# Kernel tuning notes

Hardware: AMD Instinct MI355X
Metric: run time of the kernel (lower is better)

Reference implementation:

```python
import jax, jax.numpy as jnp
import numpy as np

V, D, T, H, L, NC = 50257, 1024, 512, 16, 4, 3
HS = D // H  # head size 64
DFF = 4 * D
B = 16


def _ln(x, g, b, eps=1e-5):
    mu = jnp.mean(x, axis=-1, keepdims=True)
    var = jnp.var(x, axis=-1, keepdims=True)
    return (x - mu) * jax.lax.rsqrt(var + eps) * g + b


def setup_inputs() -> dict:
    key = jax.random.key(0)
    ks = jax.random.split(key, 20)
    s = 0.02
    inp = {
        "x": jax.random.randint(ks[0], (B, T), 0, V),
        "tok_emb": jax.random.normal(ks[1], (V, D), jnp.float32) * s,
        "pos_emb": jax.random.normal(ks[2], (T, D), jnp.float32) * s,
        "Wq": jax.random.normal(ks[3], (L, H, D, HS), jnp.float32) * s,
        "Wk": jax.random.normal(ks[4], (L, H, D, HS), jnp.float32) * s,
        "Wv": jax.random.normal(ks[5], (L, H, D, HS), jnp.float32) * s,
        "Wproj": jax.random.normal(ks[6], (L, H * HS, D), jnp.float32) * s,
        "bproj": jnp.zeros((L, D), jnp.float32),
        "ln1_g": jnp.ones((L, D), jnp.float32),
        "ln1_b": jnp.zeros((L, D), jnp.float32),
        "ln2_g": jnp.ones((L, D), jnp.float32),
        "ln2_b": jnp.zeros((L, D), jnp.float32),
        "W1": jax.random.normal(ks[7], (L, D, DFF), jnp.float32) * s,
        "b1": jnp.zeros((L, DFF), jnp.float32),
        "W2": jax.random.normal(ks[8], (L, DFF, D), jnp.float32) * s,
        "b2": jnp.zeros((L, D), jnp.float32),
        "lnf_g": jnp.ones((D,), jnp.float32),
        "lnf_b": jnp.zeros((D,), jnp.float32),
        "Wout": jax.random.normal(ks[9], (T * D, NC), jnp.float32) * s,
        "bout": jnp.zeros((NC,), jnp.float32),
    }
    return inp


def reference(x, tok_emb, pos_emb, Wq, Wk, Wv, Wproj, bproj, ln1_g, ln1_b,
              ln2_g, ln2_b, W1, b1, W2, b2, lnf_g, lnf_b, Wout, bout):
    Bx, Tx = x.shape
    h = tok_emb[x] + pos_emb[:Tx]  # [B,T,D]; dropout=identity (eval)
    scale = HS ** -0.5
    for l in range(L):
        z = _ln(h, ln1_g[l], ln1_b[l])
        q = jnp.einsum('btd,hde->bhte', z, Wq[l])
        k = jnp.einsum('btd,hde->bhte', z, Wk[l])
        v = jnp.einsum('btd,hde->bhte', z, Wv[l])
        att = jax.nn.softmax(jnp.einsum('bhte,bhse->bhts', q, k) * scale, axis=-1)
        o = jnp.einsum('bhts,bhse->bhte', att, v)  # [B,H,T,HS]
        o = o.transpose(0, 2, 1, 3).reshape(Bx, Tx, H * HS)
        h = h + o @ Wproj[l] + bproj[l]
        z2 = _ln(h, ln2_g[l], ln2_b[l])
        ffn = jax.nn.gelu(z2 @ W1[l] + b1[l], approximate=False) @ W2[l] + b2[l]
        h = h + ffn
    h = _ln(h, lnf_g, lnf_b)
    logits = h.reshape(Bx, -1) @ Wout + bout  # [B,NC]
    return logits
```

## Files before the change

kernel.cpp:

```cpp
#include <hip/hip_runtime.h>
#include <math.h>
#include <stdint.h>

#define DEV __device__ __forceinline__

constexpr int Bz = 16, T = 512, D = 1024, H = 16, HS = 64, Lx = 4, DFF = 4096, NCn = 3;
constexpr int BT = Bz * T;
constexpr long QSZ = (long)Bz * H * T * HS;

typedef __attribute__((ext_vector_type(8))) short v8s;
typedef __attribute__((ext_vector_type(4))) float v4f;

DEV uint16_t f2bf(float f) {
  uint32_t u = __float_as_uint(f);
  u += 0x7fff + ((u >> 16) & 1);
  return (uint16_t)(u >> 16);
}

DEV void async_copy16(const void* g, void* l) {
  __builtin_amdgcn_global_load_lds(
      (const __attribute__((address_space(1))) uint32_t*)g,
      (__attribute__((address_space(3))) uint32_t*)l, 16, 0, 0);
}

__global__ void transpose_cast_kernel(const float* __restrict__ in, uint16_t* __restrict__ out,
                                      int R, int C, long s1, long s2, int zdiv) {
  __shared__ float tile[32][33];
  int zz = blockIdx.z;
  in += (long)zz * R * C;
  out += (long)(zz / zdiv) * s1 + (long)(zz % zdiv) * s2;
  int c0 = blockIdx.x * 32, r0 = blockIdx.y * 32;
  int tx = threadIdx.x, ty = threadIdx.y;
  for (int i = 0; i < 32; i += 8)
    tile[ty + i][tx] = in[(long)(r0 + ty + i) * C + (c0 + tx)];
  __syncthreads();
  for (int i = 0; i < 32; i += 8)
    out[(long)(c0 + ty + i) * R + (r0 + tx)] = f2bf(tile[tx][ty + i]);
}

__global__ void embed_kernel(const int* __restrict__ x, const float* __restrict__ tok,
                             const float* __restrict__ pos, float* __restrict__ h) {
  int row = blockIdx.x;
  int t = row & (T - 1);
  int id = x[row];
  const float4* tr = (const float4*)(tok + (long)id * D);
  const float4* pr = (const float4*)(pos + (long)t * D);
  float4* hr = (float4*)(h + (long)row * D);
  int i = threadIdx.x;
  float4 a = tr[i], b = pr[i];
  hr[i] = make_float4(a.x + b.x, a.y + b.y, a.z + b.z, a.w + b.w);
}

template <bool OUT_BF16>
__global__ void ln_kernel(const float* __restrict__ in, const float* __restrict__ g,
                          const float* __restrict__ b, void* __restrict__ out) {
  int row = blockIdx.x;
  int i = threadIdx.x;
  const float4* xr = (const float4*)(in + (long)row * D);
  float4 v = xr[i];
  float s = v.x + v.y + v.z + v.w;
  float s2 = v.x * v.x + v.y * v.y + v.z * v.z + v.w * v.w;
  for (int off = 32; off; off >>= 1) { s += __shfl_down(s, off); s2 += __shfl_down(s2, off); }
  __shared__ float sh1[4], sh2[4];
  int wid = i >> 6, lane = i & 63;
  if (lane == 0) { sh1[wid] = s; sh2[wid] = s2; }
  __syncthreads();
  s = sh1[0] + sh1[1] + sh1[2] + sh1[3];
  s2 = sh2[0] + sh2[1] + sh2[2] + sh2[3];
  float mu = s * (1.0f / D);
  float rstd = rsqrtf(s2 * (1.0f / D) - mu * mu + 1e-5f);
  float4 gv = ((const float4*)g)[i];
  float4 bv = ((const float4*)b)[i];
  float o0 = (v.x - mu) * rstd * gv.x + bv.x;
  float o1 = (v.y - mu) * rstd * gv.y + bv.y;
  float o2 = (v.z - mu) * rstd * gv.z + bv.z;
  float o3 = (v.w - mu) * rstd * gv.w + bv.w;
  if constexpr (OUT_BF16) {
    uint16_t* orow = (uint16_t*)out + (long)row * D;
    orow[4 * i + 0] = f2bf(o0); orow[4 * i + 1] = f2bf(o1);
    orow[4 * i + 2] = f2bf(o2); orow[4 * i + 3] = f2bf(o3);
  } else {
    ((float4*)((float*)out + (long)row * D))[i] = make_float4(o0, o1, o2, o3);
  }
}

__global__ void softmax_kernel(uint16_t* __restrict__ S) {
  int wid = threadIdx.x >> 6, lane = threadIdx.x & 63;
  long row = (long)blockIdx.x * 4 + wid;
  uint4* p = (uint4*)(S + row * T) + lane;
  uint4 u = *p;
  uint32_t w[4] = {u.x, u.y, u.z, u.w};
  float lo[4], hi[4];
  float m = -1e30f;
#pragma unroll
  for (int i = 0; i < 4; i++) {
    lo[i] = __uint_as_float(w[i] << 16) * 0.125f;
    hi[i] = __uint_as_float(w[i] & 0xffff0000u) * 0.125f;
    m = fmaxf(m, fmaxf(lo[i], hi[i]));
  }
  for (int off = 32; off; off >>= 1) m = fmaxf(m, __shfl_xor(m, off));
  float s = 0.f;
#pragma unroll
  for (int i = 0; i < 4; i++) {
    lo[i] = expf(lo[i] - m); hi[i] = expf(hi[i] - m);
    s += lo[i] + hi[i];
  }
  for (int off = 32; off; off >>= 1) s += __shfl_xor(s, off);
  float inv = 1.0f / s;
  uint4 o;
  uint32_t* ow = (uint32_t*)&o;
#pragma unroll
  for (int i = 0; i < 4; i++)
    ow[i] = (uint32_t)f2bf(lo[i] * inv) | ((uint32_t)f2bf(hi[i] * inv) << 16);
  *p = o;
}

enum { MQKV = 0, MBF = 1, MO = 2, MATOMIC = 3, MGELU = 4 };

template <int BM, int BN, int WGM, int WGN, int MODE>
__global__ void gemm_kernel(const uint16_t* __restrict__ A, const uint16_t* __restrict__ Bt,
                            int M, int N, int K, int lda, int ldb,
                            long strideA, long strideB, long strideC,
                            const float* __restrict__ bias, void* __restrict__ Cout) {
  constexpr int WM = BM / WGM, WN = BN / WGN;
  constexpr int TM = WM / 16, TN = WN / 16;
  __shared__ __align__(16) uint16_t As[2][BM * 32];
  __shared__ __align__(16) uint16_t Bs[2][BN * 32];
  int kz = 0, batch = 0;
  if constexpr (MODE == MATOMIC) kz = blockIdx.z; else batch = blockIdx.z;
  A += (long)batch * strideA;
  Bt += (long)batch * strideB;
  const int kb0 = kz * K;
  int bm0 = blockIdx.x * BM, bn0 = blockIdx.y * BN;
  int tid = threadIdx.x, wid = tid >> 6, lane = tid & 63;
  int wm = wid / WGN, wn = wid % WGN;
  v4f acc[TM][TN] = {};

  const int laneRow = lane >> 2;
  const int laneB = ((lane & 3) ^ ((laneRow >> 1) & 3)) * 16;
  const int rl = lane & 15;
  const int cx16 = (rl * 4 + ((lane >> 4) ^ ((rl >> 1) & 3))) * 16;

  for (int k0 = kb0; k0 < kb0 + K; k0 += 64) {
    __syncthreads();
#pragma unroll
    for (int p = 0; p < 2; p++) {
      for (int c = wid; c < BM / 16; c += 4) {
        int row = bm0 + c * 16 + laneRow;
        async_copy16((const char*)(A + (long)row * lda + k0 + p * 32) + laneB,
                     (char*)As[p] + c * 1024);
      }
      for (int c = wid; c < BN / 16; c += 4) {
        int col = bn0 + c * 16 + laneRow;
        async_copy16((const char*)(Bt + (long)col * ldb + k0 + p * 32) + laneB,
                     (char*)Bs[p] + c * 1024);
      }
    }
    __syncthreads();

#pragma unroll
    for (int p = 0; p < 2; p++) {
      v8s af[TM], bfr[TN];
#pragma unroll
      for (int i = 0; i < TM; i++)
        af[i] = *(const v8s*)((const char*)As[p] + (wm * (WM / 16) + i) * 1024 + cx16);
#pragma unroll
      for (int j = 0; j < TN; j++)
        bfr[j] = *(const v8s*)((const char*)Bs[p] + (wn * (WN / 16) + j) * 1024 + cx16);
#pragma unroll
      for (int i = 0; i < TM; i++)
#pragma unroll
        for (int j = 0; j < TN; j++)
          acc[i][j] = __builtin_amdgcn_mfma_f32_16x16x32_bf16(af[i], bfr[j], acc[i][j], 0, 0, 0);
    }
  }

#pragma unroll
  for (int i = 0; i < TM; i++) {
    int row0 = bm0 + wm * WM + i * 16 + (lane >> 4) * 4;
#pragma unroll
    for (int j = 0; j < TN; j++) {
      int col = bn0 + wn * WN + j * 16 + (lane & 15);
#pragma unroll
      for (int r = 0; r < 4; r++) {
        int row = row0 + r;
        float val = acc[i][j][r];
        if constexpr (MODE == MQKV) {
          int sel = col >> 10, c = col & 1023;
          int hh = c >> 6, e = c & 63;
          int b = row >> 9, t = row & 511;
          long idx = (sel < 2) ? (((long)(b * H + hh) * T + t) * HS + e)
                               : (((long)(b * H + hh) * HS + e) * T + t);
          ((uint16_t*)Cout)[(long)sel * QSZ + idx] = f2bf(val);
        } else if constexpr (MODE == MBF) {
          ((uint16_t*)Cout)[(long)batch * strideC + (long)row * N + col] = f2bf(val);
        } else if constexpr (MODE == MO) {
          int b = batch >> 4, hh = batch & 15;
          ((uint16_t*)Cout)[((long)(b * T + row) * H + hh) * HS + col] = f2bf(val);
        } else if constexpr (MODE == MATOMIC) {
          float add = val + ((kz == 0) ? bias[col] : 0.f);
          atomicAdd(&((float*)Cout)[(long)row * N + col], add);
        } else if constexpr (MODE == MGELU) {
          float xg = val + bias[col];
          float gl = 0.5f * xg * (1.0f + erff(xg * 0.70710678118f));
          ((uint16_t*)Cout)[(long)row * N + col] = f2bf(gl);
        }
      }
    }
  }
}

__global__ void logits_init(const float* __restrict__ bout, float* __restrict__ out) {
  int i = threadIdx.x;
  if (i < Bz * NCn) out[i] = bout[i % NCn];
}
__global__ void logits_kernel(const float* __restrict__ hf, const float* __restrict__ Wout,
                              float* __restrict__ out) {
  int b = blockIdx.y, c = blockIdx.z;
  long base = (long)blockIdx.x * 8192;
  const float* hv = hf + (long)b * T * D + base;
  const float* w = Wout + base * NCn + c;
  float s = 0.f;
  for (int i = threadIdx.x; i < 8192; i += 256) s += hv[i] * w[(long)i * NCn];
  for (int off = 32; off; off >>= 1) s += __shfl_down(s, off);
  __shared__ float sh[4];
  int wid = threadIdx.x >> 6, lane = threadIdx.x & 63;
  if (lane == 0) sh[wid] = s;
  __syncthreads();
  if (threadIdx.x == 0) atomicAdd(out + b * NCn + c, sh[0] + sh[1] + sh[2] + sh[3]);
}

extern "C" void kernel_launch(void* const* d_in, const int* in_sizes, int n_in,
                              void* d_out, int out_size, void* d_ws, size_t ws_size,
                              hipStream_t stream) {
  const int* x = (const int*)d_in[0];
  const float* tok = (const float*)d_in[1];
  const float* pos = (const float*)d_in[2];
  const float* Wq = (const float*)d_in[3];
  const float* Wk = (const float*)d_in[4];
  const float* Wv = (const float*)d_in[5];
  const float* Wproj = (const float*)d_in[6];
  const float* bproj = (const float*)d_in[7];
  const float* ln1g = (const float*)d_in[8];
  const float* ln1b = (const float*)d_in[9];
  const float* ln2g = (const float*)d_in[10];
  const float* ln2b = (const float*)d_in[11];
  const float* W1 = (const float*)d_in[12];
  const float* b1 = (const float*)d_in[13];
  const float* W2 = (const float*)d_in[14];
  const float* b2 = (const float*)d_in[15];
  const float* lnfg = (const float*)d_in[16];
  const float* lnfb = (const float*)d_in[17];
  const float* Wout = (const float*)d_in[18];
  const float* bout = (const float*)d_in[19];
  float* out = (float*)d_out;

  char* ws = (char*)d_ws;
  size_t off = 0;
  auto alloc = [&](size_t bytes) { char* p = ws + off; off += (bytes + 255) & ~(size_t)255; return p; };
  uint16_t* wqkvT = (uint16_t*)alloc((size_t)Lx * 3 * D * D * 2);
  uint16_t* wpT = (uint16_t*)alloc((size_t)Lx * D * D * 2);
  uint16_t* w1T = (uint16_t*)alloc((size_t)Lx * D * DFF * 2);
  uint16_t* w2T = (uint16_t*)alloc((size_t)Lx * D * DFF * 2);
  float* h = (float*)alloc((size_t)BT * D * 4);
  uint16_t* z = (uint16_t*)alloc((size_t)BT * D * 2);
  uint16_t* qkv = (uint16_t*)alloc((size_t)3 * QSZ * 2);
  uint16_t* Sb = (uint16_t*)alloc((size_t)Bz * H * T * T * 2);
  uint16_t* o = (uint16_t*)alloc((size_t)BT * D * 2);
  uint16_t* a1 = (uint16_t*)alloc((size_t)BT * DFF * 2);
  (void)ws_size; (void)in_sizes; (void)n_in; (void)out_size;

  uint16_t* q = qkv;
  uint16_t* kb = qkv + QSZ;
  uint16_t* vt = qkv + 2 * QSZ;

  dim3 tb(32, 8);
  transpose_cast_kernel<<<dim3(HS / 32, D / 32, Lx * H), tb, 0, stream>>>(
      Wq, wqkvT, D, HS, 3L * D * D, (long)HS * D, H);
  transpose_cast_kernel<<<dim3(HS / 32, D / 32, Lx * H), tb, 0, stream>>>(
      Wk, wqkvT + (long)D * D, D, HS, 3L * D * D, (long)HS * D, H);
  transpose_cast_kernel<<<dim3(HS / 32, D / 32, Lx * H), tb, 0, stream>>>(
      Wv, wqkvT + 2L * D * D, D, HS, 3L * D * D, (long)HS * D, H);
  transpose_cast_kernel<<<dim3(D / 32, D / 32, Lx), tb, 0, stream>>>(
      Wproj, wpT, D, D, (long)D * D, 0, 1);
  transpose_cast_kernel<<<dim3(DFF / 32, D / 32, Lx), tb, 0, stream>>>(
      W1, w1T, D, DFF, (long)D * DFF, 0, 1);
  transpose_cast_kernel<<<dim3(D / 32, DFF / 32, Lx), tb, 0, stream>>>(
      W2, w2T, DFF, D, (long)D * DFF, 0, 1);

  embed_kernel<<<BT, 256, 0, stream>>>(x, tok, pos, h);

  for (int l = 0; l < Lx; l++) {
    const uint16_t* wqkv_l = wqkvT + (size_t)l * 3 * D * D;
    const uint16_t* wp_l = wpT + (size_t)l * D * D;
    const uint16_t* w1_l = w1T + (size_t)l * D * DFF;
    const uint16_t* w2_l = w2T + (size_t)l * D * DFF;

    ln_kernel<true><<<BT, 256, 0, stream>>>(h, ln1g + l * D, ln1b + l * D, z);

    gemm_kernel<128, 128, 2, 2, MQKV><<<dim3(BT / 128, 3 * D / 128, 1), 256, 0, stream>>>(
        z, wqkv_l, BT, 3 * D, D, D, D, 0, 0, 0, nullptr, qkv);

    gemm_kernel<128, 128, 2, 2, MBF><<<dim3(T / 128, T / 128, Bz * H), 256, 0, stream>>>(
        q, kb, T, T, HS, HS, HS, (long)T * HS, (long)T * HS, (long)T * T, nullptr, Sb);

    softmax_kernel<<<Bz * H * T / 4, 256, 0, stream>>>(Sb);

    gemm_kernel<128, 64, 4, 1, MO><<<dim3(T / 128, 1, Bz * H), 256, 0, stream>>>(
        Sb, vt, T, HS, T, T, T, (long)T * T, (long)HS * T, 0, nullptr, o);

    gemm_kernel<128, 128, 2, 2, MATOMIC><<<dim3(BT / 128, D / 128, 2), 256, 0, stream>>>(
        o, wp_l, BT, D, D / 2, D, D, 0, 0, 0, bproj + l * D, h);

    ln_kernel<true><<<BT, 256, 0, stream>>>(h, ln2g + l * D, ln2b + l * D, z);

    gemm_kernel<128, 128, 2, 2, MGELU><<<dim3(BT / 128, DFF / 128, 1), 256, 0, stream>>>(
        z, w1_l, BT, DFF, D, D, D, 0, 0, 0, b1 + l * DFF, a1);

    gemm_kernel<128, 128, 2, 2, MATOMIC><<<dim3(BT / 128, D / 128, 2), 256, 0, stream>>>(
        a1, w2_l, BT, D, DFF / 2, DFF, DFF, 0, 0, 0, b2 + l * D, h);
  }

  ln_kernel<false><<<BT, 256, 0, stream>>>(h, lnfg, lnfb, h);
  logits_init<<<1, 64, 0, stream>>>(bout, out);
  logits_kernel<<<dim3(64, Bz, NCn), 256, 0, stream>>>(h, Wout, out);
}
```

Baseline: 2.484 ms.

## Add 256x256 tiled 8-wave GEMM with XCD-aware remap for dense projections

Introduces a new GEMM kernel with 256x256 output tiles and 512 threads per block. It uses double-buffered async global-to-LDS copies with swizzled layout and splits each K-step into four MFMA phases interleaved with prefetch stages and priority hints. Block IDs are remapped so that neighbouring tiles land on the same XCD. The QKV, output projection and both FFN GEMMs now use it, aiming for more data reuse per tile and better L2 locality. The trade-off is a large register and LDS footprint per block and fewer blocks, which may lower occupancy or leave CUs idle on the smaller N=1024 GEMMs.

After: 2.696 ms. +8.6%, slower.

```diff
diff --git a/kernel.cpp b/kernel.cpp
--- a/kernel.cpp
+++ b/kernel.cpp
@@ -185,18 +185,167 @@
       for (int r = 0; r < 4; r++) {
         int row = row0 + r;
         float val = acc[i][j][r];
-        if constexpr (MODE == MQKV) {
-          int sel = col >> 10, c = col & 1023;
-          int hh = c >> 6, e = c & 63;
-          int b = row >> 9, t = row & 511;
-          long idx = (sel < 2) ? (((long)(b * H + hh) * T + t) * HS + e)
-                               : (((long)(b * H + hh) * HS + e) * T + t);
-          ((uint16_t*)Cout)[(long)sel * QSZ + idx] = f2bf(val);
-        } else if constexpr (MODE == MBF) {
+        if constexpr (MODE == MBF) {
           ((uint16_t*)Cout)[(long)batch * strideC + (long)row * N + col] = f2bf(val);
         } else if constexpr (MODE == MO) {
           int b = batch >> 4, hh = batch & 15;
           ((uint16_t*)Cout)[((long)(b * T + row) * H + hh) * HS + col] = f2bf(val);
+        }
+      }
+    }
+  }
+}
+
+template <int MODE>
+__global__ __launch_bounds__(512, 2) void gemm256_kernel(
+    const uint16_t* __restrict__ A, const uint16_t* __restrict__ Bt,
+    int mt, int N, int K, int lda, int ldb,
+    const float* __restrict__ bias, void* __restrict__ Cout) {
+  __shared__ __align__(16) uint16_t lds[8][8192];
+  const int NT = K >> 6;
+  int kz = 0;
+  if constexpr (MODE == MATOMIC) kz = blockIdx.z;
+  const int kb0 = kz * K;
+
+  int nwg = gridDim.x, orig = blockIdx.x;
+  int q = nwg >> 3, r = nwg & 7;
+  int xcd = orig & 7, base = orig >> 3;
+  int wgid = (xcd < r ? xcd * (q + 1) : r * (q + 1) + (xcd - r) * q) + base;
+  int bm0 = (wgid % mt) * 256, bn0 = (wgid / mt) * 256;
+
+  int tid = threadIdx.x, wid = tid >> 6, lane = tid & 63;
+  int wm = wid >> 2, wn = wid & 3;
+
+  const int laneRow = lane >> 2;
+  const int g8 = ((lane & 3) ^ ((laneRow >> 1) & 3)) * 8;
+  const int rl = lane & 15;
+  const int cx16 = (rl * 4 + ((lane >> 4) ^ ((rl >> 1) & 3))) * 16;
+
+  auto stage = [&](int h) {
+    if (h >= 4 * NT) return;
+    int th = h >> 2, part = h & 3;
+    char* slot = (char*)lds[(th & 1) * 4 + part];
+    int k0 = kb0 + th * 64;
+    const uint16_t* src; int ld, r0;
+    if (part < 2) { src = Bt; ld = ldb; r0 = bn0 + part * 128; }
+    else          { src = A;  ld = lda; r0 = bm0 + (part - 2) * 128; }
+#pragma unroll
+    for (int c0 = 0; c0 < 2; c0++) {
+      int c = wid + c0 * 8;
+      int rg = c >> 1, kc = c & 1;
+      async_copy16(src + (long)(r0 + rg * 16 + laneRow) * ld + k0 + kc * 32 + g8,
+                   slot + c * 1024);
+    }
+  };
+
+  v4f acc[8][4] = {};
+
+  for (int h = 0; h < 6; h++) stage(h);
+  asm volatile("s_waitcnt vmcnt(4)" ::: "memory");
+  __builtin_amdgcn_s_barrier();
+
+  for (int t = 0; t < NT; t++) {
+    const char* Aslot = (const char*)lds[(t & 1) * 4 + 2 + wm];
+    const char* Bslot = (const char*)lds[(t & 1) * 4 + (wn >> 1)];
+    const int jb = (wn & 1) * 4;
+    v8s af[4][2], bf0[2][2], bf1[2][2];
+
+#pragma unroll
+    for (int i = 0; i < 4; i++)
+#pragma unroll
+      for (int kc = 0; kc < 2; kc++)
+        af[i][kc] = *(const v8s*)(Aslot + (i * 2 + kc) * 1024 + cx16);
+#pragma unroll
+    for (int j = 0; j < 2; j++)
+#pragma unroll
+      for (int kc = 0; kc < 2; kc++)
+        bf0[j][kc] = *(const v8s*)(Bslot + ((jb + j) * 2 + kc) * 1024 + cx16);
+    stage(4 * t + 6);
+    __builtin_amdgcn_s_barrier();
+    asm volatile("s_waitcnt lgkmcnt(0)" ::: "memory");
+    __builtin_amdgcn_s_setprio(1);
+#pragma unroll
+    for (int i = 0; i < 4; i++)
+#pragma unroll
+      for (int j = 0; j < 2; j++)
+#pragma unroll
+        for (int kc = 0; kc < 2; kc++)
+          acc[i][j] = __builtin_amdgcn_mfma_f32_16x16x32_bf16(af[i][kc], bf0[j][kc], acc[i][j], 0, 0, 0);
+    __builtin_amdgcn_s_setprio(0);
+    __builtin_amdgcn_s_barrier();
+
+#pragma unroll
+    for (int j = 0; j < 2; j++)
+#pragma unroll
+      for (int kc = 0; kc < 2; kc++)
+        bf1[j][kc] = *(const v8s*)(Bslot + ((jb + 2 + j) * 2 + kc) * 1024 + cx16);
+    stage(4 * t + 7);
+    __builtin_amdgcn_s_barrier();
+    asm volatile("s_waitcnt lgkmcnt(0)" ::: "memory");
+    __builtin_amdgcn_s_setprio(1);
+#pragma unroll
+    for (int i = 0; i < 4; i++)
+#pragma unroll
+      for (int j = 0; j < 2; j++)
+#pragma unroll
+        for (int kc = 0; kc < 2; kc++)
+          acc[i][2 + j] = __builtin_amdgcn_mfma_f32_16x16x32_bf16(af[i][kc], bf1[j][kc], acc[i][2 + j], 0, 0, 0);
+    __builtin_amdgcn_s_setprio(0);
+    __builtin_amdgcn_s_barrier();
+
+#pragma unroll
+    for (int i = 0; i < 4; i++)
+#pragma unroll
+      for (int kc = 0; kc < 2; kc++)
+        af[i][kc] = *(const v8s*)(Aslot + ((4 + i) * 2 + kc) * 1024 + cx16);
+    stage(4 * t + 8);
+    __builtin_amdgcn_s_barrier();
+    asm volatile("s_waitcnt lgkmcnt(0)" ::: "memory");
+    __builtin_amdgcn_s_setprio(1);
+#pragma unroll
+    for (int i = 0; i < 4; i++)
+#pragma unroll
+      for (int j = 0; j < 2; j++)
+#pragma unroll
+        for (int kc = 0; kc < 2; kc++)
+          acc[4 + i][2 + j] = __builtin_amdgcn_mfma_f32_16x16x32_bf16(af[i][kc], bf1[j][kc], acc[4 + i][2 + j], 0, 0, 0);
+    __builtin_amdgcn_s_setprio(0);
+    __builtin_amdgcn_s_barrier();
+
+    stage(4 * t + 9);
+    if (t >= NT - 2) asm volatile("s_waitcnt vmcnt(0)" ::: "memory");
+    else             asm volatile("s_waitcnt vmcnt(4)" ::: "memory");
+    __builtin_amdgcn_s_barrier();
+    asm volatile("s_waitcnt lgkmcnt(0)" ::: "memory");
+    __builtin_amdgcn_s_setprio(1);
+#pragma unroll
+    for (int i = 0; i < 4; i++)
+#pragma unroll
+      for (int j = 0; j < 2; j++)
+#pragma unroll
+        for (int kc = 0; kc < 2; kc++)
+          acc[4 + i][j] = __builtin_amdgcn_mfma_f32_16x16x32_bf16(af[i][kc], bf0[j][kc], acc[4 + i][j], 0, 0, 0);
+    __builtin_amdgcn_s_setprio(0);
+    __builtin_amdgcn_s_barrier();
+  }
+
+#pragma unroll
+  for (int i = 0; i < 8; i++) {
+    int row0 = bm0 + wm * 128 + i * 16 + (lane >> 4) * 4;
+#pragma unroll
+    for (int j = 0; j < 4; j++) {
+      int col = bn0 + wn * 64 + j * 16 + rl;
+#pragma unroll
+      for (int r = 0; r < 4; r++) {
+        int row = row0 + r;
+        float val = acc[i][j][r];
+        if constexpr (MODE == MQKV) {
+          int sel = col >> 10, c = col & 1023;
+          int hh = c >> 6, e = c & 63;
+          int b = row >> 9, tt = row & 511;
+          long idx = (sel < 2) ? (((long)(b * H + hh) * T + tt) * HS + e)
+                               : (((long)(b * H + hh) * HS + e) * T + tt);
+          ((uint16_t*)Cout)[(long)sel * QSZ + idx] = f2bf(val);
         } else if constexpr (MODE == MATOMIC) {
           float add = val + ((kz == 0) ? bias[col] : 0.f);
           atomicAdd(&((float*)Cout)[(long)row * N + col], add);
@@ -290,6 +439,8 @@
 
   embed_kernel<<<BT, 256, 0, stream>>>(x, tok, pos, h);
 
+  constexpr int MT = BT / 256;
+
   for (int l = 0; l < Lx; l++) {
     const uint16_t* wqkv_l = wqkvT + (size_t)l * 3 * D * D;
     const uint16_t* wp_l = wpT + (size_t)l * D * D;
@@ -298,8 +449,8 @@
 
     ln_kernel<true><<<BT, 256, 0, stream>>>(h, ln1g + l * D, ln1b + l * D, z);
 
-    gemm_kernel<128, 128, 2, 2, MQKV><<<dim3(BT / 128, 3 * D / 128, 1), 256, 0, stream>>>(
-        z, wqkv_l, BT, 3 * D, D, D, D, 0, 0, 0, nullptr, qkv);
+    gemm256_kernel<MQKV><<<dim3(MT * (3 * D / 256), 1, 1), 512, 0, stream>>>(
+        z, wqkv_l, MT, 3 * D, D, D, D, nullptr, qkv);
 
     gemm_kernel<128, 128, 2, 2, MBF><<<dim3(T / 128, T / 128, Bz * H), 256, 0, stream>>>(
         q, kb, T, T, HS, HS, HS, (long)T * HS, (long)T * HS, (long)T * T, nullptr, Sb);
@@ -309,16 +460,16 @@
     gemm_kernel<128, 64, 4, 1, MO><<<dim3(T / 128, 1, Bz * H), 256, 0, stream>>>(
         Sb, vt, T, HS, T, T, T, (long)T * T, (long)HS * T, 0, nullptr, o);
 
-    gemm_kernel<128, 128, 2, 2, MATOMIC><<<dim3(BT / 128, D / 128, 2), 256, 0, stream>>>(
-        o, wp_l, BT, D, D / 2, D, D, 0, 0, 0, bproj + l * D, h);
+    gemm256_kernel<MATOMIC><<<dim3(MT * (D / 256), 1, 2), 512, 0, stream>>>(
+        o, wp_l, MT, D, D / 2, D, D, bproj + l * D, h);
 
     ln_kernel<true><<<BT, 256, 0, stream>>>(h, ln2g + l * D, ln2b + l * D, z);
 
-    gemm_kernel<128, 128, 2, 2, MGELU><<<dim3(BT / 128, DFF / 128, 1), 256, 0, stream>>>(
-        z, w1_l, BT, DFF, D, D, D, 0, 0, 0, b1 + l * DFF, a1);
-
-    gemm_kernel<128, 128, 2, 2, MATOMIC><<<dim3(BT / 128, D / 128, 2), 256, 0, stream>>>(
-        a1, w2_l, BT, D, DFF / 2, DFF, DFF, 0, 0, 0, b2 + l * D, h);
+    gemm256_kernel<MGELU><<<dim3(MT * (DFF / 256), 1, 1), 512, 0, stream>>>(
+        z, w1_l, MT, DFF, D, D, D, b1 + l * DFF, a1);
+
+    gemm256_kernel<MATOMIC><<<dim3(MT * (D / 256), 1, 2), 512, 0, stream>>>(
+        a1, w2_l, MT, D, DFF / 2, DFF, DFF, b2 + l * D, h);
   }
 
   ln_kernel<false><<<BT, 256, 0, stream>>>(h, lnfg, lnfb, h);
```
